# Optimization experiments

Hardware: AMD Instinct MI355X
Metric: run time of the kernel (lower is better)

The kernel has to match this reference:

```python
import jax, jax.numpy as jnp
import numpy as np

POOLED_SIZES = [11, 8, 6, 4]
Q_POOLED = 2
NUM_HEADS = 2
EPS_ROUND = 1e-3  # module's self.eps used only in aspect-ratio rounding
LN_EPS = 1e-5     # torch nn.LayerNorm default


def _pool_mat(in_size, out_size):
    # PyTorch adaptive_avg_pool1d windows: start=floor(i*in/out), end=ceil((i+1)*in/out)
    M = np.zeros((out_size, in_size), np.float32)
    for i in range(out_size):
        s = (i * in_size) // out_size
        e = -(((-(i + 1)) * in_size) // out_size)
        M[i, s:e] = 1.0 / (e - s)
    return jnp.asarray(M)


def _bilinear_mat(in_size, out_size):
    # PyTorch F.interpolate bilinear, align_corners=False (half-pixel centers, clamped)
    scale = in_size / out_size
    M = np.zeros((out_size, in_size), np.float32)
    for i in range(out_size):
        src = (i + 0.5) * scale - 0.5
        src = min(max(src, 0.0), in_size - 1)
        i0 = int(np.floor(src))
        i1 = min(i0 + 1, in_size - 1)
        w = src - i0
        M[i, i0] += 1.0 - w
        M[i, i1] += w
    return jnp.asarray(M)


def _ln(x, g, b):
    m = jnp.mean(x, axis=-1, keepdims=True)
    v = jnp.mean((x - m) ** 2, axis=-1, keepdims=True)
    return (x - m) * jax.lax.rsqrt(v + LN_EPS) * g + b


def _out_size(p, H, W):
    if W >= H:
        return (p, round(W * p / H + EPS_ROUND))
    return (round(H * p / W + EPS_ROUND), p)


def setup_inputs() -> dict:
    key = jax.random.key(0)
    ks = jax.random.split(key, 12)
    B, C, H, W = 8, 32, 512, 512
    L = len(POOLED_SIZES)
    return {
        "x": jax.random.normal(ks[0], (B, C, H, W), jnp.float32),
        "q_w": jax.random.normal(ks[1], (C, C), jnp.float32) * 0.05,
        "q_b": jax.random.normal(ks[2], (C,), jnp.float32) * 0.01,
        "kv_w": jax.random.normal(ks[3], (C, 2 * C), jnp.float32) * 0.05,
        "kv_b": jax.random.normal(ks[4], (2 * C,), jnp.float32) * 0.01,
        "proj_w": jax.random.normal(ks[5], (C, C), jnp.float32) * 0.05,
        "proj_b": jax.random.normal(ks[6], (C,), jnp.float32) * 0.01,
        "norm_g": jnp.ones((C,), jnp.float32),
        "norm_b": jnp.zeros((C,), jnp.float32),
        "dconv_w": jax.random.normal(ks[7], (L, C, 1, 3, 3), jnp.float32) * 0.05,  # OIHW depthwise, stacked per level
        "dconv_b": jax.random.normal(ks[8], (L, C), jnp.float32) * 0.01,
        "H": 512,
        "W": 512,
    }


def reference(x, q_w, q_b, kv_w, kv_b, proj_w, proj_b, norm_g, norm_b, dconv_w, dconv_b, H, W):
    B, C = x.shape[0], x.shape[1]
    nh = NUM_HEADS
    hd = C // nh
    scale = hd ** (-0.5)

    # ---- query branch: adaptive pool to ~2x2, then linear ----
    qh, qw = _out_size(Q_POOLED, H, W)
    qp = jnp.einsum('ph,bchw,qw->bcpq', _pool_mat(H, qh), x, _pool_mat(W, qw))  # (B,C,qh,qw)
    qt = qp.reshape(B, C, -1).transpose(0, 2, 1)                               # (B,Nq,C)
    q = (qt @ q_w + q_b).reshape(B, -1, nh, hd).transpose(0, 2, 1, 3)          # (B,nh,Nq,hd)

    # ---- KV pyramid: adaptive pool + depthwise conv residual per level ----
    toks = []
    for i, p in enumerate(POOLED_SIZES):
        ph, pw = _out_size(p, H, W)
        pooled = jnp.einsum('ph,bchw,qw->bcpq', _pool_mat(H, ph), x, _pool_mat(W, pw))
        conv = jax.lax.conv_general_dilated(
            pooled, dconv_w[i], window_strides=(1, 1), padding='SAME',
            feature_group_count=C, dimension_numbers=('NCHW', 'OIHW', 'NCHW'))
        conv = conv + dconv_b[i][None, :, None, None]
        toks.append((pooled + conv).reshape(B, C, -1))
    toks = jnp.concatenate(toks, axis=2).transpose(0, 2, 1)  # (B,Nk,C), Nk=237
    toks = _ln(toks, norm_g, norm_b)

    kv = (toks @ kv_w + kv_b).reshape(B, -1, 2, nh, hd).transpose(2, 0, 3, 1, 4)
    k, v = kv[0], kv[1]                                       # (B,nh,Nk,hd)

    # ---- small-scale attention ----
    attn = jax.nn.softmax(jnp.einsum('bhqd,bhkd->bhqk', q, k) * scale, axis=-1)
    o = jnp.einsum('bhqk,bhkd->bhqd', attn, v).transpose(0, 2, 1, 3).reshape(B, -1, C)
    o = o @ proj_w + proj_b                                    # (B,Nq,C)

    # ---- bilinear upsample back to (H,W) ----
    o = o.transpose(0, 2, 1).reshape(B, C, qh, qw)
    out = jnp.einsum('hp,bcpq,wq->bchw', _bilinear_mat(qh, H), o, _bilinear_mat(qw, W))
    return out  # (B,C,H,W), same as module's to_4d output
```

## Files before the change

kernel.cpp:

```cpp
#include <hip/hip_runtime.h>
#include <math.h>

#define BB 8
#define CC 32
#define NTOK 241
#define NKV 237
#define YPADW 516
#define NSLOT 16

struct Win { int idx, s, e, left; float acc; };

template <int P, int SBASE>
__device__ __forceinline__ void wstep(Win& w, int nown, float v, int r,
                                      float* __restrict__ Y, int c) {
  if (w.left > 0) {
    w.acc += (r >= w.s) ? v : 0.0f;
    if (r == w.e - 1) {
      Y[(SBASE + (nown - w.left)) * YPADW + c] = w.acc;
      w.left--;
      w.idx++;
      int sn = (w.idx * 512) / P;
      w.acc = (sn <= r) ? v : 0.0f;
      w.s = sn;
      w.e = ((w.idx + 1) * 512 + P - 1) / P;
    }
  }
}

template <int P>
__device__ __forceinline__ void winit(Win& w, int i0, int n) {
  w.idx = i0;
  w.s = (i0 * 512) / P;
  w.e = ((i0 + 1) * 512 + P - 1) / P;
  w.left = n;
  w.acc = 0.0f;
}

__global__ __launch_bounds__(512) void pool_kernel(const float* __restrict__ x,
                                                   float* __restrict__ pooled) {
  __shared__ float sh[8 * 512];
  __shared__ float Ybuf[NSLOT * YPADW];

  const int plane = blockIdx.x >> 1;
  const int q = blockIdx.x & 1;
  const int tid = threadIdx.x;
  const int c = tid;

  const int lo = q ? 256 : 0;
  const int nb = q ? 32 : 35;
  int i0_2, n_2, i0_11, n_11, i0_8, n_8, i0_6, n_6, i0_4, n_4;
  if (q == 0) {
    i0_2 = 0; n_2 = 1; i0_11 = 0; n_11 = 6; i0_8 = 0; n_8 = 4;
    i0_6 = 0; n_6 = 3; i0_4 = 0; n_4 = 2;
  } else {
    i0_2 = 1; n_2 = 1; i0_11 = 6; n_11 = 5; i0_8 = 4; n_8 = 4;
    i0_6 = 3; n_6 = 3; i0_4 = 2; n_4 = 2;
  }

  Win W2, W11, W8, W6, W4;
  winit<2>(W2, i0_2, n_2);
  winit<11>(W11, i0_11, n_11);
  winit<8>(W8, i0_8, n_8);
  winit<6>(W6, i0_6, n_6);
  winit<4>(W4, i0_4, n_4);

  const float* xp = x + (size_t)plane * (512 * 512);
  const int row0 = tid >> 7;
  const int cg = (tid & 127) * 4;

  float4 r0 = *(const float4*)(xp + (size_t)(lo + row0) * 512 + cg);
  float4 r1 = *(const float4*)(xp + (size_t)(lo + row0 + 4) * 512 + cg);

  for (int band = 0; band < nb; ++band) {
    *(float4*)(sh + row0 * 512 + cg) = r0;
    *(float4*)(sh + (row0 + 4) * 512 + cg) = r1;
    __syncthreads();
    if (band + 1 < nb) {
      int rb = lo + (band + 1) * 8;
      r0 = *(const float4*)(xp + (size_t)(rb + row0) * 512 + cg);
      r1 = *(const float4*)(xp + (size_t)(rb + row0 + 4) * 512 + cg);
    }
#pragma unroll
    for (int rr = 0; rr < 8; ++rr) {
      float v = sh[rr * 512 + c];
      int r = lo + band * 8 + rr;
      wstep<2, 0>(W2, n_2, v, r, Ybuf, c);
      wstep<11, 1>(W11, n_11, v, r, Ybuf, c);
      wstep<8, 7>(W8, n_8, v, r, Ybuf, c);
      wstep<6, 11>(W6, n_6, v, r, Ybuf, c);
      wstep<4, 14>(W4, n_4, v, r, Ybuf, c);
    }
    __syncthreads();
  }

  const int Ps[5]  = {2, 11, 8, 6, 4};
  const int KBs[5] = {0, 4, 125, 189, 225};
  const int SBs[5] = {0, 1, 7, 11, 14};
  const int i0s[5] = {i0_2, i0_11, i0_8, i0_6, i0_4};
  const int ns[5]  = {n_2, n_11, n_8, n_6, n_4};
  int cum[6]; cum[0] = 0;
#pragma unroll
  for (int l = 0; l < 5; ++l) cum[l + 1] = cum[l] + ns[l] * Ps[l];

  if (tid < cum[5]) {
    int l = 0;
    while (tid >= cum[l + 1]) ++l;
    int P = Ps[l];
    int rel = tid - cum[l];
    int li = rel / P, j = rel - li * P;
    int i = i0s[l] + li;
    int s = (i * 512) / P, e = ((i + 1) * 512 + P - 1) / P;
    int sw = (j * 512) / P, ew = ((j + 1) * 512 + P - 1) / P;
    const float* row = &Ybuf[(SBs[l] + li) * YPADW];
    float t0 = 0.f, t1 = 0.f, t2 = 0.f, t3 = 0.f;
    int cc = sw;
    for (; cc + 4 <= ew; cc += 4) {
      t0 += row[cc]; t1 += row[cc + 1]; t2 += row[cc + 2]; t3 += row[cc + 3];
    }
    for (; cc < ew; ++cc) t0 += row[cc];
    float val = ((t0 + t1) + (t2 + t3)) / (float)((e - s) * (ew - sw));
    pooled[(size_t)plane * NTOK + KBs[l] + i * P + j] = val;
  }
}

__global__ __launch_bounds__(512) void attn_kernel(
    const float* __restrict__ pooled,
    const float* __restrict__ q_w, const float* __restrict__ q_b,
    const float* __restrict__ kv_w, const float* __restrict__ kv_b,
    const float* __restrict__ proj_w, const float* __restrict__ proj_b,
    const float* __restrict__ norm_g, const float* __restrict__ norm_b,
    const float* __restrict__ dconv_w, const float* __restrict__ dconv_b,
    float* __restrict__ o_out) {
  __shared__ float pl[CC * NTOK];
  __shared__ float toks[NKV][33];
  __shared__ float kvls[NKV][65];
  __shared__ float kvw[CC * 64];
  __shared__ float dw[4 * CC * 9];
  __shared__ float dbias[4 * CC];
  __shared__ float qbias[CC], kvb[64], gln[CC], bln[CC];
  __shared__ float qtok[4][CC];
  __shared__ float attno[4][33];

  const int b = blockIdx.x, tid = threadIdx.x;
  const float* plg = pooled + (size_t)b * CC * NTOK;
  for (int i = tid; i < CC * NTOK; i += 512) pl[i] = plg[i];
  for (int i = tid; i < CC * 64; i += 512) kvw[i] = kv_w[i];
  for (int i = tid; i < 4 * CC * 9; i += 512) dw[i] = dconv_w[i];
  if (tid < 4 * CC) dbias[tid] = dconv_b[tid];
  if (tid < CC) { qbias[tid] = q_b[tid]; gln[tid] = norm_g[tid]; bln[tid] = norm_b[tid]; }
  if (tid >= 64 && tid < 128) kvb[tid - 64] = kv_b[tid - 64];
  __syncthreads();

  for (int item = tid; item < NKV * CC; item += 512) {
    int t = item >> 5, c = item & 31;
    int l, p, kb_, tb;
    if (t < 121)      { l = 0; p = 11; kb_ = 4;   tb = 0; }
    else if (t < 185) { l = 1; p = 8;  kb_ = 125; tb = 121; }
    else if (t < 221) { l = 2; p = 6;  kb_ = 189; tb = 185; }
    else              { l = 3; p = 4;  kb_ = 225; tb = 221; }
    int ti = t - tb;
    int i = ti / p, j = ti - i * p;
    const float* plc = pl + c * NTOK + kb_;
    const float* w9 = dw + (l * CC + c) * 9;
    float acc = dbias[l * CC + c];
#pragma unroll
    for (int dy = -1; dy <= 1; ++dy)
#pragma unroll
      for (int dx = -1; dx <= 1; ++dx) {
        int ii = i + dy, jj = j + dx;
        if (ii >= 0 && ii < p && jj >= 0 && jj < p)
          acc += w9[(dy + 1) * 3 + (dx + 1)] * plc[ii * p + jj];
      }
    toks[t][c] = plc[i * p + j] + acc;
  }
  __syncthreads();

  if (tid < NKV) {
    float xv[32]; float m = 0.f;
#pragma unroll
    for (int c = 0; c < 32; ++c) { xv[c] = toks[tid][c]; m += xv[c]; }
    m *= (1.0f / 32.0f);
    float v = 0.f;
#pragma unroll
    for (int c = 0; c < 32; ++c) { float d = xv[c] - m; v += d * d; }
    v *= (1.0f / 32.0f);
    float rs = rsqrtf(v + 1e-5f);
#pragma unroll
    for (int c = 0; c < 32; ++c) toks[tid][c] = (xv[c] - m) * rs * gln[c] + bln[c];
  } else if (tid >= 384) {
    int it = tid - 384;
    int n = it >> 5, u = it & 31;
    float acc = qbias[u];
#pragma unroll
    for (int c = 0; c < 32; ++c) acc += pl[c * NTOK + n] * q_w[c * 32 + u];
    qtok[n][u] = acc * 0.25f;
  }
  __syncthreads();

  for (int item = tid; item < NKV * 64; item += 512) {
    int t = item >> 6, u = item & 63;
    float acc = kvb[u];
#pragma unroll
    for (int c = 0; c < 32; ++c) acc += toks[t][c] * kvw[c * 64 + u];
    kvls[t][u] = acc;
  }
  __syncthreads();

  {
    int wave = tid >> 6, lane = tid & 63;
    int h = wave >> 2, qi = wave & 3;
    float qv[16];
#pragma unroll
    for (int d = 0; d < 16; ++d) qv[d] = qtok[qi][h * 16 + d];
    float sc[4];
#pragma unroll
    for (int m = 0; m < 4; ++m) {
      int t = lane + m * 64;
      float s = -1e30f;
      if (t < NKV) {
        s = 0.f;
#pragma unroll
        for (int d = 0; d < 16; ++d) s += qv[d] * kvls[t][h * 16 + d];
      }
      sc[m] = s;
    }
    float mx = fmaxf(fmaxf(sc[0], sc[1]), fmaxf(sc[2], sc[3]));
#pragma unroll
    for (int d = 1; d < 64; d <<= 1) mx = fmaxf(mx, __shfl_xor(mx, d));
    float pr[4]; float ssum = 0.f;
#pragma unroll
    for (int m = 0; m < 4; ++m) {
      int t = lane + m * 64;
      pr[m] = (t < NKV) ? expf(sc[m] - mx) : 0.0f;
      ssum += pr[m];
    }
#pragma unroll
    for (int d = 1; d < 64; d <<= 1) ssum += __shfl_xor(ssum, d);
    float acc[16];
#pragma unroll
    for (int d = 0; d < 16; ++d) acc[d] = 0.f;
#pragma unroll
    for (int m = 0; m < 4; ++m) {
      int t = lane + m * 64;
      if (t < NKV) {
        float p = pr[m];
#pragma unroll
        for (int d = 0; d < 16; ++d) acc[d] += p * kvls[t][32 + h * 16 + d];
      }
    }
#pragma unroll
    for (int d = 0; d < 16; ++d) {
#pragma unroll
      for (int s = 1; s < 64; s <<= 1) acc[d] += __shfl_xor(acc[d], s);
    }
    if (lane == 0) {
      float inv = 1.0f / ssum;
#pragma unroll
      for (int d = 0; d < 16; ++d) attno[qi][h * 16 + d] = acc[d] * inv;
    }
  }
  __syncthreads();

  if (tid < 128) {
    int n = tid >> 5, u = tid & 31;
    float acc = proj_b[u];
#pragma unroll
    for (int c = 0; c < 32; ++c) acc += attno[n][c] * proj_w[c * 32 + u];
    o_out[((size_t)b * 32 + u) * 4 + n] = acc;
  }
}

__global__ __launch_bounds__(256) void upsample_kernel(const float* __restrict__ o_in,
                                                       float* __restrict__ out) {
  const int plane = blockIdx.x >> 3;
  const int chunk = blockIdx.x & 7;
  const int tid = threadIdx.x;
  const int sub = tid >> 7, col4 = tid & 127;

  const float o00 = o_in[plane * 4 + 0];
  const float o01 = o_in[plane * 4 + 1];
  const float o10 = o_in[plane * 4 + 2];
  const float o11 = o_in[plane * 4 + 3];

  float top[4], bot[4];
#pragma unroll
  for (int k = 0; k < 4; ++k) {
    float c = (float)(4 * col4 + k) + 0.5f;
    float ww = c * (1.0f / 256.0f) - 0.5f;
    ww = fminf(fmaxf(ww, 0.0f), 1.0f);
    top[k] = o00 + ww * (o01 - o00);
    bot[k] = o10 + ww * (o11 - o10);
  }
  float* outp = out + (size_t)plane * (512 * 512);
  const int r0 = chunk * 64;
  for (int i = 0; i < 32; ++i) {
    int r = r0 + 2 * i + sub;
    float wh = ((float)r + 0.5f) * (1.0f / 256.0f) - 0.5f;
    wh = fminf(fmaxf(wh, 0.0f), 1.0f);
    float4 v;
    v.x = top[0] + wh * (bot[0] - top[0]);
    v.y = top[1] + wh * (bot[1] - top[1]);
    v.z = top[2] + wh * (bot[2] - top[2]);
    v.w = top[3] + wh * (bot[3] - top[3]);
    *(float4*)(outp + r * 512 + 4 * col4) = v;
  }
}

extern "C" void kernel_launch(void* const* d_in, const int* in_sizes, int n_in,
                              void* d_out, int out_size, void* d_ws, size_t ws_size,
                              hipStream_t stream) {
  const float* x       = (const float*)d_in[0];
  const float* q_w     = (const float*)d_in[1];
  const float* q_b     = (const float*)d_in[2];
  const float* kv_w    = (const float*)d_in[3];
  const float* kv_b    = (const float*)d_in[4];
  const float* proj_w  = (const float*)d_in[5];
  const float* proj_b  = (const float*)d_in[6];
  const float* norm_g  = (const float*)d_in[7];
  const float* norm_b  = (const float*)d_in[8];
  const float* dconv_w = (const float*)d_in[9];
  const float* dconv_b = (const float*)d_in[10];
  float* out = (float*)d_out;

  float* pooled = (float*)d_ws;
  float* o_ws   = pooled + (size_t)BB * CC * NTOK;

  pool_kernel<<<BB * CC * 2, 512, 0, stream>>>(x, pooled);
  attn_kernel<<<BB, 512, 0, stream>>>(pooled, q_w, q_b, kv_w, kv_b, proj_w,
                                      proj_b, norm_g, norm_b, dconv_w, dconv_b,
                                      o_ws);
  upsample_kernel<<<BB * CC * 8, 256, 0, stream>>>(o_ws, out);
}
```

Measured before the change: 210.4 us.

## Stream rows directly into per-thread float4 window accumulators with shared atomics

The pooling kernel no longer stages 8-row bands through shared memory with two barriers per band. Each thread now owns a 4-column group and one of every four rows, keeping float4 window accumulators in registers. Partial column sums are merged into a zero-initialised shared buffer with atomicAdd, and four loads are kept in flight through a rotating register prefetch. This removes the per-band barriers and the shared-memory round trip, at the cost of shared atomics, a buffer zeroing pass and extra clamped loads past the last row.

```diff
diff --git a/kernel.cpp b/kernel.cpp
--- a/kernel.cpp
+++ b/kernel.cpp
@@ -5,49 +5,57 @@
 #define CC 32
 #define NTOK 241
 #define NKV 237
-#define YPADW 516
+#define YW 516
 #define NSLOT 16
 
-struct Win { int idx, s, e, left; float acc; };
-
-template <int P, int SBASE>
-__device__ __forceinline__ void wstep(Win& w, int nown, float v, int r,
-                                      float* __restrict__ Y, int c) {
-  if (w.left > 0) {
-    w.acc += (r >= w.s) ? v : 0.0f;
-    if (r == w.e - 1) {
-      Y[(SBASE + (nown - w.left)) * YPADW + c] = w.acc;
-      w.left--;
-      w.idx++;
-      int sn = (w.idx * 512) / P;
-      w.acc = (sn <= r) ? v : 0.0f;
-      w.s = sn;
-      w.e = ((w.idx + 1) * 512 + P - 1) / P;
-    }
-  }
-}
+struct WS { int idx, s, e, left, slot; float ax, ay, az, aw; };
 
 template <int P>
-__device__ __forceinline__ void winit(Win& w, int i0, int n) {
+__device__ __forceinline__ void ws_init(WS& w, int i0, int n, int sb) {
   w.idx = i0;
   w.s = (i0 * 512) / P;
   w.e = ((i0 + 1) * 512 + P - 1) / P;
   w.left = n;
-  w.acc = 0.0f;
+  w.slot = sb;
+  w.ax = w.ay = w.az = w.aw = 0.f;
+}
+
+template <int P>
+__device__ __forceinline__ void ws_step(WS& w, float4 v, int r,
+                                        float* __restrict__ Y, int c4) {
+  if (w.left > 0) {
+    if (r >= w.s && r < w.e) {
+      w.ax += v.x; w.ay += v.y; w.az += v.z; w.aw += v.w;
+    }
+    if (r < w.e && r + 4 >= w.e) {
+      float* dst = Y + w.slot * YW + c4;
+      atomicAdd(dst + 0, w.ax);
+      atomicAdd(dst + 1, w.ay);
+      atomicAdd(dst + 2, w.az);
+      atomicAdd(dst + 3, w.aw);
+      w.slot++; w.left--; w.idx++;
+      int sn = (w.idx * 512) / P;
+      w.e = ((w.idx + 1) * 512 + P - 1) / P;
+      bool ov = (sn <= r);
+      w.ax = ov ? v.x : 0.f; w.ay = ov ? v.y : 0.f;
+      w.az = ov ? v.z : 0.f; w.aw = ov ? v.w : 0.f;
+      w.s = sn;
+    }
+  }
 }
 
 __global__ __launch_bounds__(512) void pool_kernel(const float* __restrict__ x,
                                                    float* __restrict__ pooled) {
-  __shared__ float sh[8 * 512];
-  __shared__ float Ybuf[NSLOT * YPADW];
+  __shared__ float Ybuf[NSLOT * YW];
 
   const int plane = blockIdx.x >> 1;
   const int q = blockIdx.x & 1;
   const int tid = threadIdx.x;
-  const int c = tid;
+
+  for (int i = tid; i < NSLOT * YW; i += 512) Ybuf[i] = 0.f;
 
   const int lo = q ? 256 : 0;
-  const int nb = q ? 32 : 35;
+  const int NIT = q ? 64 : 72;
   int i0_2, n_2, i0_11, n_11, i0_8, n_8, i0_6, n_6, i0_4, n_4;
   if (q == 0) {
     i0_2 = 0; n_2 = 1; i0_11 = 0; n_11 = 6; i0_8 = 0; n_8 = 4;
@@ -57,41 +65,41 @@
     i0_6 = 3; n_6 = 3; i0_4 = 2; n_4 = 2;
   }
 
-  Win W2, W11, W8, W6, W4;
-  winit<2>(W2, i0_2, n_2);
-  winit<11>(W11, i0_11, n_11);
-  winit<8>(W8, i0_8, n_8);
-  winit<6>(W6, i0_6, n_6);
-  winit<4>(W4, i0_4, n_4);
-
+  WS W2, W11, W8, W6, W4;
+  ws_init<2>(W2, i0_2, n_2, 0);
+  ws_init<11>(W11, i0_11, n_11, 1);
+  ws_init<8>(W8, i0_8, n_8, 7);
+  ws_init<6>(W6, i0_6, n_6, 11);
+  ws_init<4>(W4, i0_4, n_4, 14);
+
+  const int r0 = tid >> 7;
+  const int c4 = (tid & 127) * 4;
   const float* xp = x + (size_t)plane * (512 * 512);
-  const int row0 = tid >> 7;
-  const int cg = (tid & 127) * 4;
-
-  float4 r0 = *(const float4*)(xp + (size_t)(lo + row0) * 512 + cg);
-  float4 r1 = *(const float4*)(xp + (size_t)(lo + row0 + 4) * 512 + cg);
-
-  for (int band = 0; band < nb; ++band) {
-    *(float4*)(sh + row0 * 512 + cg) = r0;
-    *(float4*)(sh + (row0 + 4) * 512 + cg) = r1;
-    __syncthreads();
-    if (band + 1 < nb) {
-      int rb = lo + (band + 1) * 8;
-      r0 = *(const float4*)(xp + (size_t)(rb + row0) * 512 + cg);
-      r1 = *(const float4*)(xp + (size_t)(rb + row0 + 4) * 512 + cg);
-    }
-#pragma unroll
-    for (int rr = 0; rr < 8; ++rr) {
-      float v = sh[rr * 512 + c];
-      int r = lo + band * 8 + rr;
-      wstep<2, 0>(W2, n_2, v, r, Ybuf, c);
-      wstep<11, 1>(W11, n_11, v, r, Ybuf, c);
-      wstep<8, 7>(W8, n_8, v, r, Ybuf, c);
-      wstep<6, 11>(W6, n_6, v, r, Ybuf, c);
-      wstep<4, 14>(W4, n_4, v, r, Ybuf, c);
-    }
-    __syncthreads();
-  }
+
+  __syncthreads();
+
+#define LOADIT(IT) \
+  (*(const float4*)(xp + (size_t)min(lo + r0 + 4 * (IT), 511) * 512 + c4))
+#define PROCIT(V, IT)                                                          \
+  {                                                                            \
+    int r = lo + r0 + 4 * (IT);                                                \
+    ws_step<2>(W2, V, r, Ybuf, c4);                                            \
+    ws_step<11>(W11, V, r, Ybuf, c4);                                          \
+    ws_step<8>(W8, V, r, Ybuf, c4);                                            \
+    ws_step<6>(W6, V, r, Ybuf, c4);                                            \
+    ws_step<4>(W4, V, r, Ybuf, c4);                                            \
+  }
+
+  float4 Av = LOADIT(0), Bv = LOADIT(1), Cv = LOADIT(2), Dv = LOADIT(3);
+  for (int it = 0; it < NIT; it += 4) {
+    PROCIT(Av, it);     Av = LOADIT(it + 4);
+    PROCIT(Bv, it + 1); Bv = LOADIT(it + 5);
+    PROCIT(Cv, it + 2); Cv = LOADIT(it + 6);
+    PROCIT(Dv, it + 3); Dv = LOADIT(it + 7);
+  }
+#undef LOADIT
+#undef PROCIT
+  __syncthreads();
 
   const int Ps[5]  = {2, 11, 8, 6, 4};
   const int KBs[5] = {0, 4, 125, 189, 225};
@@ -111,7 +119,7 @@
     int i = i0s[l] + li;
     int s = (i * 512) / P, e = ((i + 1) * 512 + P - 1) / P;
     int sw = (j * 512) / P, ew = ((j + 1) * 512 + P - 1) / P;
-    const float* row = &Ybuf[(SBs[l] + li) * YPADW];
+    const float* row = &Ybuf[(SBs[l] + li) * YW];
     float t0 = 0.f, t1 = 0.f, t2 = 0.f, t3 = 0.f;
     int cc = sw;
     for (; cc + 4 <= ew; cc += 4) {
```

Measured after the change: 222.4 us. 5.7% more time.

## Split pooling into 4-row partial-sum pass plus per-level window kernel; flatten upsample grid

Applied to the files above, without the earlier changes.

Replaces the single 512-block streaming pool kernel with two kernels. The first reduces each plane into 4-row group sums using 16384 blocks. The second, one block per plane and level, builds each row window from those group sums plus leftover raw rows, then sums across columns. The goal is to spread the 256 MB read of x across many more blocks than the old 512-block grid, at the cost of writing and rereading a 64 MB intermediate and needing that workspace (with a fallback to the old kernel). The upsample kernel is also changed to one row pair per block over 65536 blocks, raising parallelism but dropping the per-thread reuse of the horizontal interpolation.

```diff
diff --git a/kernel.cpp b/kernel.cpp
--- a/kernel.cpp
+++ b/kernel.cpp
@@ -5,8 +5,70 @@
 #define CC 32
 #define NTOK 241
 #define NKV 237
-#define YPADW 516
-#define NSLOT 16
+
+__global__ __launch_bounds__(256) void g4_kernel(const float* __restrict__ x,
+                                                 float* __restrict__ G4) {
+  const int b = blockIdx.x;
+  const int plane = b >> 6, band = b & 63;
+  const int t = threadIdx.x;
+  const int gh = t >> 7;
+  const int c4 = (t & 127) * 4;
+  const float* xp = x + (size_t)plane * (512 * 512) + (size_t)(band * 8 + gh * 4) * 512 + c4;
+  float4 a0 = *(const float4*)(xp);
+  float4 a1 = *(const float4*)(xp + 512);
+  float4 a2 = *(const float4*)(xp + 1024);
+  float4 a3 = *(const float4*)(xp + 1536);
+  float4 s;
+  s.x = (a0.x + a1.x) + (a2.x + a3.x);
+  s.y = (a0.y + a1.y) + (a2.y + a3.y);
+  s.z = (a0.z + a1.z) + (a2.z + a3.z);
+  s.w = (a0.w + a1.w) + (a2.w + a3.w);
+  *(float4*)(G4 + ((size_t)plane * 128 + band * 2 + gh) * 512 + c4) = s;
+}
+
+__global__ __launch_bounds__(512) void win_kernel(const float* __restrict__ x,
+                                                  const float* __restrict__ G4,
+                                                  float* __restrict__ pooled) {
+  __shared__ float Y[11][520];
+  const int b = blockIdx.x;
+  const int plane = b / 5, lvl = b - plane * 5;
+  const int Ps[5]  = {2, 11, 8, 6, 4};
+  const int KBs[5] = {0, 4, 125, 189, 225};
+  const int p = Ps[lvl], kb = KBs[lvl];
+  const int col = threadIdx.x;
+  const float* xp = x + (size_t)plane * (512 * 512);
+  const float* g4 = G4 + (size_t)plane * 128 * 512;
+
+  for (int i = 0; i < p; ++i) {
+    int s = (i * 512) / p, e = ((i + 1) * 512 + p - 1) / p;
+    int gs = (s + 3) >> 2, ge = e >> 2;
+    float sum = 0.f;
+    for (int r = s; r < gs * 4; ++r) sum += xp[(size_t)r * 512 + col];
+    float s0 = 0.f, s1 = 0.f;
+    int g = gs;
+    for (; g + 2 <= ge; g += 2) {
+      s0 += g4[(size_t)g * 512 + col];
+      s1 += g4[(size_t)(g + 1) * 512 + col];
+    }
+    if (g < ge) s0 += g4[(size_t)g * 512 + col];
+    sum += s0 + s1;
+    for (int r = ge * 4; r < e; ++r) sum += xp[(size_t)r * 512 + col];
+    Y[i][col] = sum;
+  }
+  __syncthreads();
+
+  if (col < p * p) {
+    int i = col / p, j = col - i * p;
+    int s = (i * 512) / p, e = ((i + 1) * 512 + p - 1) / p;
+    int sw = (j * 512) / p, ew = ((j + 1) * 512 + p - 1) / p;
+    float t0 = 0.f, t1 = 0.f;
+    int c = sw;
+    for (; c + 2 <= ew; c += 2) { t0 += Y[i][c]; t1 += Y[i][c + 1]; }
+    if (c < ew) t0 += Y[i][c];
+    pooled[(size_t)plane * NTOK + kb + i * p + j] =
+        (t0 + t1) / (float)((e - s) * (ew - sw));
+  }
+}
 
 struct Win { int idx, s, e, left; float acc; };
 
@@ -16,9 +78,8 @@
   if (w.left > 0) {
     w.acc += (r >= w.s) ? v : 0.0f;
     if (r == w.e - 1) {
-      Y[(SBASE + (nown - w.left)) * YPADW + c] = w.acc;
-      w.left--;
-      w.idx++;
+      Y[(SBASE + (nown - w.left)) * 516 + c] = w.acc;
+      w.left--; w.idx++;
       int sn = (w.idx * 512) / P;
       w.acc = (sn <= r) ? v : 0.0f;
       w.s = sn;
@@ -36,41 +97,27 @@
   w.acc = 0.0f;
 }
 
-__global__ __launch_bounds__(512) void pool_kernel(const float* __restrict__ x,
-                                                   float* __restrict__ pooled) {
+__global__ __launch_bounds__(512) void pool_fb(const float* __restrict__ x,
+                                               float* __restrict__ pooled) {
   __shared__ float sh[8 * 512];
-  __shared__ float Ybuf[NSLOT * YPADW];
-
+  __shared__ float Ybuf[16 * 516];
   const int plane = blockIdx.x >> 1;
   const int q = blockIdx.x & 1;
   const int tid = threadIdx.x;
   const int c = tid;
-
   const int lo = q ? 256 : 0;
   const int nb = q ? 32 : 35;
   int i0_2, n_2, i0_11, n_11, i0_8, n_8, i0_6, n_6, i0_4, n_4;
-  if (q == 0) {
-    i0_2 = 0; n_2 = 1; i0_11 = 0; n_11 = 6; i0_8 = 0; n_8 = 4;
-    i0_6 = 0; n_6 = 3; i0_4 = 0; n_4 = 2;
-  } else {
-    i0_2 = 1; n_2 = 1; i0_11 = 6; n_11 = 5; i0_8 = 4; n_8 = 4;
-    i0_6 = 3; n_6 = 3; i0_4 = 2; n_4 = 2;
-  }
-
+  if (q == 0) { i0_2 = 0; n_2 = 1; i0_11 = 0; n_11 = 6; i0_8 = 0; n_8 = 4; i0_6 = 0; n_6 = 3; i0_4 = 0; n_4 = 2; }
+  else        { i0_2 = 1; n_2 = 1; i0_11 = 6; n_11 = 5; i0_8 = 4; n_8 = 4; i0_6 = 3; n_6 = 3; i0_4 = 2; n_4 = 2; }
   Win W2, W11, W8, W6, W4;
-  winit<2>(W2, i0_2, n_2);
-  winit<11>(W11, i0_11, n_11);
-  winit<8>(W8, i0_8, n_8);
-  winit<6>(W6, i0_6, n_6);
-  winit<4>(W4, i0_4, n_4);
-
+  winit<2>(W2, i0_2, n_2); winit<11>(W11, i0_11, n_11); winit<8>(W8, i0_8, n_8);
+  winit<6>(W6, i0_6, n_6); winit<4>(W4, i0_4, n_4);
   const float* xp = x + (size_t)plane * (512 * 512);
   const int row0 = tid >> 7;
   const int cg = (tid & 127) * 4;
-
   float4 r0 = *(const float4*)(xp + (size_t)(lo + row0) * 512 + cg);
   float4 r1 = *(const float4*)(xp + (size_t)(lo + row0 + 4) * 512 + cg);
-
   for (int band = 0; band < nb; ++band) {
     *(float4*)(sh + row0 * 512 + cg) = r0;
     *(float4*)(sh + (row0 + 4) * 512 + cg) = r1;
@@ -92,7 +139,6 @@
     }
     __syncthreads();
   }
-
   const int Ps[5]  = {2, 11, 8, 6, 4};
   const int KBs[5] = {0, 4, 125, 189, 225};
   const int SBs[5] = {0, 1, 7, 11, 14};
@@ -101,7 +147,6 @@
   int cum[6]; cum[0] = 0;
 #pragma unroll
   for (int l = 0; l < 5; ++l) cum[l + 1] = cum[l] + ns[l] * Ps[l];
-
   if (tid < cum[5]) {
     int l = 0;
     while (tid >= cum[l + 1]) ++l;
@@ -111,7 +156,7 @@
     int i = i0s[l] + li;
     int s = (i * 512) / P, e = ((i + 1) * 512 + P - 1) / P;
     int sw = (j * 512) / P, ew = ((j + 1) * 512 + P - 1) / P;
-    const float* row = &Ybuf[(SBs[l] + li) * YPADW];
+    const float* row = &Ybuf[(SBs[l] + li) * 516];
     float t0 = 0.f, t1 = 0.f, t2 = 0.f, t3 = 0.f;
     int cc = sw;
     for (; cc + 4 <= ew; cc += 4) {
@@ -272,38 +317,25 @@
 
 __global__ __launch_bounds__(256) void upsample_kernel(const float* __restrict__ o_in,
                                                        float* __restrict__ out) {
-  const int plane = blockIdx.x >> 3;
-  const int chunk = blockIdx.x & 7;
-  const int tid = threadIdx.x;
-  const int sub = tid >> 7, col4 = tid & 127;
-
-  const float o00 = o_in[plane * 4 + 0];
-  const float o01 = o_in[plane * 4 + 1];
-  const float o10 = o_in[plane * 4 + 2];
-  const float o11 = o_in[plane * 4 + 3];
-
-  float top[4], bot[4];
+  const int b = blockIdx.x;
+  const int plane = b >> 8, rp = b & 255;
+  const int t = threadIdx.x;
+  const int r = rp * 2 + (t >> 7);
+  const int c4 = (t & 127) * 4;
+  const float4 o = *(const float4*)(o_in + (size_t)plane * 4);
+  float wh = ((float)r + 0.5f) * (1.0f / 256.0f) - 0.5f;
+  wh = fminf(fmaxf(wh, 0.0f), 1.0f);
+  float4 v;
+  float* vv = &v.x;
 #pragma unroll
   for (int k = 0; k < 4; ++k) {
-    float c = (float)(4 * col4 + k) + 0.5f;
-    float ww = c * (1.0f / 256.0f) - 0.5f;
+    float ww = ((float)(c4 + k) + 0.5f) * (1.0f / 256.0f) - 0.5f;
     ww = fminf(fmaxf(ww, 0.0f), 1.0f);
-    top[k] = o00 + ww * (o01 - o00);
-    bot[k] = o10 + ww * (o11 - o10);
-  }
-  float* outp = out + (size_t)plane * (512 * 512);
-  const int r0 = chunk * 64;
-  for (int i = 0; i < 32; ++i) {
-    int r = r0 + 2 * i + sub;
-    float wh = ((float)r + 0.5f) * (1.0f / 256.0f) - 0.5f;
-    wh = fminf(fmaxf(wh, 0.0f), 1.0f);
-    float4 v;
-    v.x = top[0] + wh * (bot[0] - top[0]);
-    v.y = top[1] + wh * (bot[1] - top[1]);
-    v.z = top[2] + wh * (bot[2] - top[2]);
-    v.w = top[3] + wh * (bot[3] - top[3]);
-    *(float4*)(outp + r * 512 + 4 * col4) = v;
-  }
+    float top = o.x + ww * (o.y - o.x);
+    float bot = o.z + ww * (o.w - o.z);
+    vv[k] = top + wh * (bot - top);
+  }
+  *(float4*)(out + (size_t)plane * (512 * 512) + (size_t)r * 512 + c4) = v;
 }
 
 extern "C" void kernel_launch(void* const* d_in, const int* in_sizes, int n_in,
@@ -324,10 +356,17 @@
 
   float* pooled = (float*)d_ws;
   float* o_ws   = pooled + (size_t)BB * CC * NTOK;
-
-  pool_kernel<<<BB * CC * 2, 512, 0, stream>>>(x, pooled);
+  float* G4     = o_ws + 1024;
+  size_t need = ((size_t)BB * CC * NTOK + 1024 + (size_t)256 * 128 * 512) * 4;
+
+  if (ws_size >= need) {
+    g4_kernel<<<16384, 256, 0, stream>>>(x, G4);
+    win_kernel<<<1280, 512, 0, stream>>>(x, G4, pooled);
+  } else {
+    pool_fb<<<BB * CC * 2, 512, 0, stream>>>(x, pooled);
+  }
   attn_kernel<<<BB, 512, 0, stream>>>(pooled, q_w, q_b, kv_w, kv_b, proj_w,
                                       proj_b, norm_g, norm_b, dconv_w, dconv_b,
                                       o_ws);
-  upsample_kernel<<<BB * CC * 8, 256, 0, stream>>>(o_ws, out);
-}
+  upsample_kernel<<<65536, 256, 0, stream>>>(o_ws, out);
+}
```

Measured after the change: 216.9 us. +3.1%, slower.
